# Kernel optimization log

Measured on AMD Instinct MI355X. Metric: run time of the kernel, lower is better.

## Reference

```python
import jax, jax.numpy as jnp
import numpy as np

EPS = 1e-5

def _bn_relu(y, mean, var, scale, bias):
    # y: (b, c, n); eval-mode batchnorm over channel axis, then ReLU
    inv = scale / jnp.sqrt(var + EPS)
    return jax.nn.relu((y - mean[None, :, None]) * inv[None, :, None] + bias[None, :, None])

def setup_inputs() -> dict:
    key = jax.random.key(0)
    ks = jax.random.split(key, 6)
    b, c, n, cr = 4, 256, 4096, 32
    inp = {
        'x': jax.random.normal(ks[0], (b, c, n), jnp.float32),
        'w_q': jax.random.normal(ks[1], (cr, c), jnp.float32) * (1.0 / np.sqrt(c)),
        'w_k': jax.random.normal(ks[2], (cr, c), jnp.float32) * (1.0 / np.sqrt(c)),
        'w_v': jax.random.normal(ks[3], (c, c), jnp.float32) * (1.0 / np.sqrt(c)),
        'bn1_scale': jnp.ones((cr,), jnp.float32), 'bn1_bias': jnp.zeros((cr,), jnp.float32),
        'bn1_mean': jnp.zeros((cr,), jnp.float32), 'bn1_var': jnp.ones((cr,), jnp.float32),
        'bn2_scale': jnp.ones((cr,), jnp.float32), 'bn2_bias': jnp.zeros((cr,), jnp.float32),
        'bn2_mean': jnp.zeros((cr,), jnp.float32), 'bn2_var': jnp.ones((cr,), jnp.float32),
        'bn3_scale': jnp.ones((c,), jnp.float32), 'bn3_bias': jnp.zeros((c,), jnp.float32),
        'bn3_mean': jnp.zeros((c,), jnp.float32), 'bn3_var': jnp.ones((c,), jnp.float32),
        'gamma': jax.random.normal(ks[4], (1,), jnp.float32),
    }
    return inp

def reference(x, w_q, w_k, w_v,
              bn1_scale, bn1_bias, bn1_mean, bn1_var,
              bn2_scale, bn2_bias, bn2_mean, bn2_var,
              bn3_scale, bn3_bias, bn3_mean, bn3_var,
              gamma):
    # x: (b, c, n). Original views as (b, c, n, 1) so width=1, height=n.
    b, c, n = x.shape
    # 1x1 conv == channel matmul, then BN+ReLU
    q = _bn_relu(jnp.einsum('oc,bcn->bon', w_q, x), bn1_mean, bn1_var, bn1_scale, bn1_bias)  # (b, c', n)
    k = _bn_relu(jnp.einsum('oc,bcn->bon', w_k, x), bn2_mean, bn2_var, bn2_scale, bn2_bias)  # (b, c', n)
    v = _bn_relu(jnp.einsum('oc,bcn->bon', w_v, x), bn3_mean, bn3_var, bn3_scale, bn3_bias)  # (b, c, n)
    # energy_H: (b, n, n) with -inf diagonal (self-attention along 'height')
    energy_h = jnp.einsum('bdi,bdj->bij', q, k)
    eye = jnp.eye(n, dtype=bool)
    energy_h = jnp.where(eye[None], -jnp.inf, energy_h)
    # energy_W: width=1 -> per-position self energy (b, n)
    energy_w = jnp.sum(q * k, axis=1)
    # softmax over concat of n H-logits and 1 W-logit
    att = jax.nn.softmax(jnp.concatenate([energy_h, energy_w[..., None]], axis=-1), axis=-1)  # (b, n, n+1)
    att_h = att[..., :n]        # (b, n, n), query i -> key j
    att_w = att[..., n]         # (b, n)
    out_h = jnp.einsum('bcj,bij->bci', v, att_h)   # aggregate values along height
    out_w = v * att_w[:, None, :]                  # width=1 self term
    out = gamma[0] * (out_h + out_w) + x
    return out
```

## Files before the change

### kernel.cpp

```cpp
#include <hip/hip_runtime.h>

#define Bb 4
#define Cc 256
#define Nn 4096
#define CR 32
#define EPS_BN 1e-5f
#define SHIFT2 28.853900817779268f
#define LOG2E  1.4426950408889634f
#define JSPLIT 4
#define JSL (Nn / JSPLIT)
#define TJ 64
#define NTILES (JSL / TJ)

typedef __attribute__((ext_vector_type(8))) short short8;
typedef __attribute__((ext_vector_type(4))) float f32x4;

__device__ inline unsigned int pk2(float a, float b) {
    __bf16 ha = (__bf16)a, hb = (__bf16)b;
    unsigned short ra = __builtin_bit_cast(unsigned short, ha);
    unsigned short rb = __builtin_bit_cast(unsigned short, hb);
    return ((unsigned int)rb << 16) | ra;
}
__device__ inline float blo(unsigned int u) { return __uint_as_float(u << 16); }
__device__ inline float bhi(unsigned int u) { return __uint_as_float(u & 0xffff0000u); }
__device__ inline float ex2(float x) { return __builtin_amdgcn_exp2f(x); }

__global__ __launch_bounds__(256) void qkv_kernel(
    const float* __restrict__ x,
    const float* __restrict__ wq, const float* __restrict__ wk, const float* __restrict__ wv,
    const float* __restrict__ bn1s, const float* __restrict__ bn1b, const float* __restrict__ bn1m, const float* __restrict__ bn1v,
    const float* __restrict__ bn2s, const float* __restrict__ bn2b, const float* __restrict__ bn2m, const float* __restrict__ bn2v,
    const float* __restrict__ bn3s, const float* __restrict__ bn3b, const float* __restrict__ bn3m, const float* __restrict__ bn3v,
    __bf16* __restrict__ Qt, __bf16* __restrict__ Kt, __bf16* __restrict__ Vb)
{
    __shared__ __align__(16) __bf16 F[16384];
    __shared__ __align__(16) float  sXf[4][32 * 40];
    __shared__ __align__(16) __bf16 sXt[4][2][32 * 40];

    const int tid = threadIdx.x;
    const int n0 = blockIdx.x * 128, g = blockIdx.y, b = blockIdx.z;
    const int lane = tid & 63, w = tid >> 6;
    const int l15 = lane & 15, l4 = lane >> 4;

    {
        int r = tid >> 2, q = tid & 3;
        int R = g * 64 + r;
        const float* src = (R < 32) ? (wq + (size_t)R * Cc)
                         : (R < 64) ? (wk + (size_t)(R - 32) * Cc)
                                    : (wv + (size_t)(R - 64) * Cc);
        int mt = r >> 4, l15r = r & 15;
#pragma unroll
        for (int u8 = 0; u8 < 8; ++u8) {
            float4 a = *(const float4*)&src[q * 64 + u8 * 8];
            float4 c2 = *(const float4*)&src[q * 64 + u8 * 8 + 4];
            uint4 p = { pk2(a.x,a.y), pk2(a.z,a.w), pk2(c2.x,c2.y), pk2(c2.z,c2.w) };
            int kc = 2 * q + (u8 >> 2), l4k = u8 & 3;
            *(uint4*)&F[(((kc * 4 + mt) * 64 + l4k * 16 + l15r)) * 8] = p;
        }
    }

    float*  sXfw  = &sXf[w][0];
    __bf16* sXtw0 = &sXt[w][0][0];
    __bf16* sXtw1 = &sXt[w][1][0];

    const int cr = lane >> 3, nq = lane & 7;
    const float* xbase = x + (size_t)(b * Cc + cr) * Nn + n0 + w * 32 + nq * 4;

    float4 xg[4];
#pragma unroll
    for (int it = 0; it < 4; ++it)
        xg[it] = *(const float4*)&xbase[(size_t)(it * 8) * Nn];

    __syncthreads();

    f32x4 acc[4][2];
#pragma unroll
    for (int mt = 0; mt < 4; ++mt)
#pragma unroll
        for (int nt = 0; nt < 2; ++nt) acc[mt][nt] = (f32x4){0.f, 0.f, 0.f, 0.f};

    for (int kc = 0; kc < 8; ++kc) {
#pragma unroll
        for (int it = 0; it < 4; ++it)
            *(float4*)&sXfw[(it * 8 + cr) * 40 + nq * 4] = xg[it];

        if (kc + 1 < 8) {
#pragma unroll
            for (int it = 0; it < 4; ++it)
                xg[it] = *(const float4*)&xbase[(size_t)((kc + 1) * 32 + it * 8) * Nn];
        }

#pragma unroll
        for (int s = 0; s < 2; ++s) {
            int n = lane & 31, c0 = (lane >> 5) * 8 + s * 16;
            float h[8], lo[8];
#pragma unroll
            for (int j = 0; j < 8; ++j) {
                float v = sXfw[(c0 + j) * 40 + n];
                float hh = (float)(__bf16)v;
                h[j] = hh; lo[j] = v - hh;
            }
            uint4 H = { pk2(h[0],h[1]), pk2(h[2],h[3]), pk2(h[4],h[5]), pk2(h[6],h[7]) };
            uint4 L = { pk2(lo[0],lo[1]), pk2(lo[2],lo[3]), pk2(lo[4],lo[5]), pk2(lo[6],lo[7]) };
            *(uint4*)&sXtw0[n * 40 + c0] = H;
            *(uint4*)&sXtw1[n * 40 + c0] = L;
        }

        short8 bh[2], bl[2];
#pragma unroll
        for (int nt = 0; nt < 2; ++nt) {
            bh[nt] = *(const short8*)&sXtw0[(nt * 16 + l15) * 40 + l4 * 8];
            bl[nt] = *(const short8*)&sXtw1[(nt * 16 + l15) * 40 + l4 * 8];
        }
#pragma unroll
        for (int mt = 0; mt < 4; ++mt) {
            short8 af = *(const short8*)&F[((kc * 4 + mt) * 64 + lane) * 8];
#pragma unroll
            for (int nt = 0; nt < 2; ++nt) {
                acc[mt][nt] = __builtin_amdgcn_mfma_f32_16x16x32_bf16(af, bh[nt], acc[mt][nt], 0, 0, 0);
                acc[mt][nt] = __builtin_amdgcn_mfma_f32_16x16x32_bf16(af, bl[nt], acc[mt][nt], 0, 0, 0);
            }
        }
    }

    if (g == 0) {
#pragma unroll
        for (int mt = 0; mt < 4; ++mt) {
            float scl[4], off[4];
#pragma unroll
            for (int r = 0; r < 4; ++r) {
                int R = mt * 16 + l4 * 4 + r;
                float s, o;
                if (R < 32) {
                    s = bn1s[R] * __frsqrt_rn(bn1v[R] + EPS_BN);
                    o = bn1b[R] - bn1m[R] * s;
                } else {
                    int row = R - 32;
                    s = bn2s[row] * __frsqrt_rn(bn2v[row] + EPS_BN);
                    o = bn2b[row] - bn2m[row] * s;
                    s *= LOG2E; o *= LOG2E;
                }
                scl[r] = s; off[r] = o;
            }
            __bf16* dst = (mt < 2) ? Qt : Kt;
            int d0 = (mt & 1) * 16 + l4 * 4;
#pragma unroll
            for (int nt = 0; nt < 2; ++nt) {
                f32x4 a = acc[mt][nt];
                float e0 = fmaxf(fmaf(a.x, scl[0], off[0]), 0.f);
                float e1 = fmaxf(fmaf(a.y, scl[1], off[1]), 0.f);
                float e2 = fmaxf(fmaf(a.z, scl[2], off[2]), 0.f);
                float e3 = fmaxf(fmaf(a.w, scl[3], off[3]), 0.f);
                uint2 p = { pk2(e0, e1), pk2(e2, e3) };
                int n = n0 + w * 32 + nt * 16 + l15;
                *(uint2*)&dst[(size_t)(b * Nn + n) * CR + d0] = p;
            }
        }
    } else {
        __bf16* oT = F;
        __syncthreads();
#pragma unroll
        for (int mt = 0; mt < 4; ++mt) {
            float scl[4], off[4];
#pragma unroll
            for (int r = 0; r < 4; ++r) {
                int row = (g - 1) * 64 + mt * 16 + l4 * 4 + r;
                float s = bn3s[row] * __frsqrt_rn(bn3v[row] + EPS_BN);
                scl[r] = s; off[r] = bn3b[row] - bn3m[row] * s;
            }
#pragma unroll
            for (int nt = 0; nt < 2; ++nt) {
                f32x4 a = acc[mt][nt];
                float e[4];
                e[0] = fmaxf(fmaf(a.x, scl[0], off[0]), 0.f);
                e[1] = fmaxf(fmaf(a.y, scl[1], off[1]), 0.f);
                e[2] = fmaxf(fmaf(a.z, scl[2], off[2]), 0.f);
                e[3] = fmaxf(fmaf(a.w, scl[3], off[3]), 0.f);
                int ncol = w * 32 + nt * 16 + l15;
#pragma unroll
                for (int r = 0; r < 4; ++r)
                    oT[(mt * 16 + l4 * 4 + r) * 136 + ncol] = (__bf16)e[r];
            }
        }
        __syncthreads();
        int rr = tid >> 2, qq = tid & 3;
        size_t vrow = (size_t)(b * Cc + (g - 1) * 64 + rr) * Nn + n0 + qq * 32;
#pragma unroll
        for (int e8 = 0; e8 < 4; ++e8)
            *(uint4*)&Vb[vrow + e8 * 8] = *(const uint4*)&oT[rr * 136 + qq * 32 + e8 * 8];
    }
}

__global__ __launch_bounds__(256) void attn_kernel(
    const __bf16* __restrict__ Qt, const __bf16* __restrict__ Kt,
    const __bf16* __restrict__ Vb,
    __bf16* __restrict__ PO, float* __restrict__ PL)
{
    __shared__ __align__(16) __bf16 sQ[64 * 40];
    __shared__ __align__(16) __bf16 sP[2][64 * 72];
    __shared__ __align__(16) float  sL[4][64];

    const int tid = threadIdx.x, lane = tid & 63, w = tid >> 6;
    const int b = blockIdx.z, js = blockIdx.y, iblk = blockIdx.x;
    const int i0 = iblk * 64;
    const int l15 = lane & 15, l4 = lane >> 4;

    {
        int i = tid >> 2, o = tid & 3;
        *(uint4*)&sQ[i * 40 + o * 8] =
            *(const uint4*)&Qt[(size_t)(b * Nn + i0 + i) * CR + o * 8];
    }
    __syncthreads();
    short8 qf[4];
#pragma unroll
    for (int it = 0; it < 4; ++it)
        qf[it] = *(const short8*)&sQ[(it * 16 + l15) * 40 + l4 * 8];

    f32x4 oacc[16];
#pragma unroll
    for (int z = 0; z < 16; ++z) oacc[z] = (f32x4){0.f, 0.f, 0.f, 0.f};
    float lp[4] = {0.f, 0.f, 0.f, 0.f};

    const size_t jb = (size_t)js * JSL;

    short8 kf = *(const short8*)&Kt[(size_t)(b * Nn + jb + 16 * w + l15) * CR + l4 * 8];

    short8 vf[8];
#pragma unroll
    for (int u = 0; u < 8; ++u) {
        int jh = u >> 2, ct = u & 3;
        int c = w * 64 + ct * 16 + l15;
        vf[u] = *(const short8*)&Vb[(size_t)(b * Cc + c) * Nn + jb + (jh * 4 + l4) * 8];
    }

#pragma unroll
    for (int it = 0; it < 4; ++it) {
        f32x4 c0 = (f32x4){0.f, 0.f, 0.f, 0.f};
        c0 = __builtin_amdgcn_mfma_f32_16x16x32_bf16(kf, qf[it], c0, 0, 0, 0);
        float e0 = ex2(c0.x - SHIFT2), e1 = ex2(c0.y - SHIFT2);
        float e2 = ex2(c0.z - SHIFT2), e3 = ex2(c0.w - SHIFT2);
        lp[it] += (e0 + e1) + (e2 + e3);
        uint2 p2 = { pk2(e0, e1), pk2(e2, e3) };
        *(uint2*)&sP[0][(it * 16 + l15) * 72 + w * 16 + l4 * 4] = p2;
    }
    kf = *(const short8*)&Kt[(size_t)(b * Nn + jb + TJ + 16 * w + l15) * CR + l4 * 8];
    __syncthreads();

    for (int t = 0; t < NTILES; ++t) {
        const size_t j0 = jb + (size_t)t * TJ;
        const __bf16* sPr = &sP[t & 1][0];
        __bf16*       sPn = &sP[(t + 1) & 1][0];

        if (t + 1 < NTILES) {
#pragma unroll
            for (int it = 0; it < 4; ++it) {
                f32x4 c0 = (f32x4){0.f, 0.f, 0.f, 0.f};
                c0 = __builtin_amdgcn_mfma_f32_16x16x32_bf16(kf, qf[it], c0, 0, 0, 0);
                float e0 = ex2(c0.x - SHIFT2), e1 = ex2(c0.y - SHIFT2);
                float e2 = ex2(c0.z - SHIFT2), e3 = ex2(c0.w - SHIFT2);
                lp[it] += (e0 + e1) + (e2 + e3);
                uint2 p2 = { pk2(e0, e1), pk2(e2, e3) };
                *(uint2*)&sPn[(it * 16 + l15) * 72 + w * 16 + l4 * 4] = p2;
            }
        }

        __builtin_amdgcn_s_setprio(1);
#pragma unroll
        for (int jh = 0; jh < 2; ++jh) {
            short8 pf[4];
#pragma unroll
            for (int it = 0; it < 4; ++it)
                pf[it] = *(const short8*)&sPr[(it * 16 + l15) * 72 + jh * 32 + l4 * 8];
#pragma unroll
            for (int ct = 0; ct < 4; ++ct) {
#pragma unroll
                for (int it = 0; it < 4; ++it)
                    oacc[it * 4 + ct] = __builtin_amdgcn_mfma_f32_16x16x32_bf16(
                        pf[it], vf[jh * 4 + ct], oacc[it * 4 + ct], 0, 0, 0);
            }
        }
        __builtin_amdgcn_s_setprio(0);

        if (t + 1 < NTILES) {
#pragma unroll
            for (int u = 0; u < 8; ++u) {
                int jh = u >> 2, ct = u & 3;
                int c = w * 64 + ct * 16 + l15;
                vf[u] = *(const short8*)&Vb[(size_t)(b * Cc + c) * Nn + j0 + TJ + (jh * 4 + l4) * 8];
            }
            if (t + 2 < NTILES)
                kf = *(const short8*)&Kt[(size_t)(b * Nn + j0 + 2 * TJ + 16 * w + l15) * CR + l4 * 8];
            __syncthreads();
        }
    }

#pragma unroll
    for (int it = 0; it < 4; ++it) {
        float v = lp[it];
        v += __shfl_xor(v, 16);
        v += __shfl_xor(v, 32);
        if (lane < 16) sL[w][it * 16 + lane] = v;
    }
    __syncthreads();
    if (tid < 64)
        PL[(size_t)(js * Bb + b) * Nn + i0 + tid] =
            sL[0][tid] + sL[1][tid] + sL[2][tid] + sL[3][tid];

    const size_t base = (size_t)((js * Bb + b) * (Nn / 64) + iblk) * 16384;
#pragma unroll
    for (int it = 0; it < 4; ++it)
#pragma unroll
        for (int ct = 0; ct < 4; ++ct) {
            f32x4 a = oacc[it * 4 + ct];
            uint2 p = { pk2(a.x, a.y), pk2(a.z, a.w) };
            *(uint2*)&PO[base + (size_t)((((w * 4 + it) * 4 + ct) * 64 + lane)) * 4] = p;
        }
}

__global__ __launch_bounds__(256) void reduce_kernel(
    const __bf16* __restrict__ PO, const float* __restrict__ PL,
    const float* __restrict__ x, const float* __restrict__ gamma,
    float* __restrict__ out)
{
    __shared__ __align__(16) float oT[64 * 68];
    __shared__ float sLinv[64];

    const int tid = threadIdx.x;
    const int iblk = blockIdx.x, wq = blockIdx.y, b = blockIdx.z;
    const int i0 = iblk * 64;
    const int lane = tid & 63, ct = tid >> 6, l15 = lane & 15, l4 = lane >> 4;

    if (tid < 64) {
        float l = 0.f;
#pragma unroll
        for (int js = 0; js < JSPLIT; ++js)
            l += PL[(size_t)(js * Bb + b) * Nn + i0 + tid];
        sLinv[tid] = 1.0f / l;
    }

    float o[4][4];
#pragma unroll
    for (int it = 0; it < 4; ++it) {
        o[it][0] = o[it][1] = o[it][2] = o[it][3] = 0.f;
#pragma unroll
        for (int js = 0; js < JSPLIT; ++js) {
            size_t base = (size_t)((js * Bb + b) * (Nn / 64) + iblk) * 16384;
            uint2 v = *(const uint2*)&PO[base + (size_t)((((wq * 4 + it) * 4 + ct) * 64 + lane)) * 4];
            o[it][0] += blo(v.x); o[it][1] += bhi(v.x);
            o[it][2] += blo(v.y); o[it][3] += bhi(v.y);
        }
    }

    const int cl = ct * 16 + l15;
#pragma unroll
    for (int it = 0; it < 4; ++it) {
        float4 t4 = { o[it][0], o[it][1], o[it][2], o[it][3] };
        *(float4*)&oT[cl * 68 + it * 16 + l4 * 4] = t4;
    }
    __syncthreads();

    const float g = gamma[0];
    const int c_l = tid >> 2, icol = (tid & 3) * 16;
    const int cg = wq * 64 + c_l;
    const size_t gb = (size_t)(b * Cc + cg) * Nn + i0 + icol;
#pragma unroll
    for (int k4 = 0; k4 < 4; ++k4) {
        float4 ov = *(const float4*)&oT[c_l * 68 + icol + k4 * 4];
        float4 li = *(const float4*)&sLinv[icol + k4 * 4];
        float4 xv = *(const float4*)&x[gb + k4 * 4];
        float4 res;
        res.x = fmaf(g, ov.x * li.x, xv.x);
        res.y = fmaf(g, ov.y * li.y, xv.y);
        res.z = fmaf(g, ov.z * li.z, xv.z);
        res.w = fmaf(g, ov.w * li.w, xv.w);
        *(float4*)&out[gb + k4 * 4] = res;
    }
}

extern "C" void kernel_launch(void* const* d_in, const int* in_sizes, int n_in,
                              void* d_out, int out_size, void* d_ws, size_t ws_size,
                              hipStream_t stream)
{
    const float* x    = (const float*)d_in[0];
    const float* wq   = (const float*)d_in[1];
    const float* wk   = (const float*)d_in[2];
    const float* wv   = (const float*)d_in[3];
    const float* bn1s = (const float*)d_in[4];
    const float* bn1b = (const float*)d_in[5];
    const float* bn1m = (const float*)d_in[6];
    const float* bn1v = (const float*)d_in[7];
    const float* bn2s = (const float*)d_in[8];
    const float* bn2b = (const float*)d_in[9];
    const float* bn2m = (const float*)d_in[10];
    const float* bn2v = (const float*)d_in[11];
    const float* bn3s = (const float*)d_in[12];
    const float* bn3b = (const float*)d_in[13];
    const float* bn3m = (const float*)d_in[14];
    const float* bn3v = (const float*)d_in[15];
    const float* gmm  = (const float*)d_in[16];
    float* out = (float*)d_out;

    char* ws = (char*)d_ws;
    __bf16* Qt  = (__bf16*)(ws);
    __bf16* Kt  = (__bf16*)(ws + (1u << 20));
    __bf16* Vb  = (__bf16*)(ws + (2u << 20));
    char*   big = ws + (10u << 20);
    __bf16* PO  = (__bf16*)big;
    float*  PL  = (float*)(big + 33554432);

    qkv_kernel<<<dim3(Nn / 128, 5, Bb), 256, 0, stream>>>(
        x, wq, wk, wv,
        bn1s, bn1b, bn1m, bn1v,
        bn2s, bn2b, bn2m, bn2v,
        bn3s, bn3b, bn3m, bn3v,
        Qt, Kt, Vb);

    attn_kernel<<<dim3(Nn / 64, JSPLIT, Bb), 256, 0, stream>>>(Qt, Kt, Vb, PO, PL);

    reduce_kernel<<<dim3(Nn / 64, 4, Bb), 256, 0, stream>>>(PO, PL, x, gmm, out);
}
```

Measured before the change: 211.8 us.

## Pre-pack weights in a separate kernel and widen V projection groups to 128 rows

Adds a small prep kernel that converts the Q/K/V weights to bf16 MFMA fragment layout once, so qkv_kernel reads the fragments directly from global memory instead of each block repacking weights into LDS. The V projection is split into two groups of 128 output rows instead of four of 64, cutting the grid from 5 to 3 groups per tile. This reduces redundant x loads and hi/lo bf16 splitting per block. In exchange it adds a kernel launch, uses more accumulator registers, leaves the Q/K group doing half the work of the V groups, and uses a larger LDS staging buffer.

```diff
diff --git a/kernel.cpp b/kernel.cpp
--- a/kernel.cpp
+++ b/kernel.cpp
@@ -25,39 +25,45 @@
 __device__ inline float bhi(unsigned int u) { return __uint_as_float(u & 0xffff0000u); }
 __device__ inline float ex2(float x) { return __builtin_amdgcn_exp2f(x); }
 
+__global__ __launch_bounds__(256) void prep_w(
+    const float* __restrict__ wq, const float* __restrict__ wk,
+    const float* __restrict__ wv, __bf16* __restrict__ Wf)
+{
+    const int r16 = blockIdx.x;
+    const int tid = threadIdx.x;
+#pragma unroll
+    for (int ss = 0; ss < 2; ++ss) {
+        int s = tid + ss * 256;
+        int kc = s >> 6, lane = s & 63;
+        int R = r16 * 16 + (lane & 15);
+        const float* src = (R < 32) ? (wq + (size_t)R * Cc)
+                         : (R < 64) ? (wk + (size_t)(R - 32) * Cc)
+                                    : (wv + (size_t)(R - 64) * Cc);
+        const float* p = src + kc * 32 + (lane >> 4) * 8;
+        float4 a = *(const float4*)p;
+        float4 c2 = *(const float4*)(p + 4);
+        uint4 pk = { pk2(a.x,a.y), pk2(a.z,a.w), pk2(c2.x,c2.y), pk2(c2.z,c2.w) };
+        *(uint4*)&Wf[(((size_t)r16 * 8 + kc) * 64 + lane) * 8] = pk;
+    }
+}
+
 __global__ __launch_bounds__(256) void qkv_kernel(
-    const float* __restrict__ x,
-    const float* __restrict__ wq, const float* __restrict__ wk, const float* __restrict__ wv,
+    const float* __restrict__ x, const __bf16* __restrict__ Wf,
     const float* __restrict__ bn1s, const float* __restrict__ bn1b, const float* __restrict__ bn1m, const float* __restrict__ bn1v,
     const float* __restrict__ bn2s, const float* __restrict__ bn2b, const float* __restrict__ bn2m, const float* __restrict__ bn2v,
     const float* __restrict__ bn3s, const float* __restrict__ bn3b, const float* __restrict__ bn3m, const float* __restrict__ bn3v,
     __bf16* __restrict__ Qt, __bf16* __restrict__ Kt, __bf16* __restrict__ Vb)
 {
-    __shared__ __align__(16) __bf16 F[16384];
     __shared__ __align__(16) float  sXf[4][32 * 40];
     __shared__ __align__(16) __bf16 sXt[4][2][32 * 40];
+    __shared__ __align__(16) __bf16 oT[128 * 136];
 
     const int tid = threadIdx.x;
     const int n0 = blockIdx.x * 128, g = blockIdx.y, b = blockIdx.z;
     const int lane = tid & 63, w = tid >> 6;
     const int l15 = lane & 15, l4 = lane >> 4;
-
-    {
-        int r = tid >> 2, q = tid & 3;
-        int R = g * 64 + r;
-        const float* src = (R < 32) ? (wq + (size_t)R * Cc)
-                         : (R < 64) ? (wk + (size_t)(R - 32) * Cc)
-                                    : (wv + (size_t)(R - 64) * Cc);
-        int mt = r >> 4, l15r = r & 15;
-#pragma unroll
-        for (int u8 = 0; u8 < 8; ++u8) {
-            float4 a = *(const float4*)&src[q * 64 + u8 * 8];
-            float4 c2 = *(const float4*)&src[q * 64 + u8 * 8 + 4];
-            uint4 p = { pk2(a.x,a.y), pk2(a.z,a.w), pk2(c2.x,c2.y), pk2(c2.z,c2.w) };
-            int kc = 2 * q + (u8 >> 2), l4k = u8 & 3;
-            *(uint4*)&F[(((kc * 4 + mt) * 64 + l4k * 16 + l15r)) * 8] = p;
-        }
-    }
+    const int nmt = (g == 0) ? 4 : 8;
+    const int r16b = (g == 0) ? 0 : 4 + (g - 1) * 8;
 
     float*  sXfw  = &sXf[w][0];
     __bf16* sXtw0 = &sXt[w][0][0];
@@ -71,11 +77,9 @@
     for (int it = 0; it < 4; ++it)
         xg[it] = *(const float4*)&xbase[(size_t)(it * 8) * Nn];
 
-    __syncthreads();
-
-    f32x4 acc[4][2];
-#pragma unroll
-    for (int mt = 0; mt < 4; ++mt)
+    f32x4 acc[8][2];
+#pragma unroll
+    for (int mt = 0; mt < 8; ++mt)
 #pragma unroll
         for (int nt = 0; nt < 2; ++nt) acc[mt][nt] = (f32x4){0.f, 0.f, 0.f, 0.f};
 
@@ -112,13 +116,19 @@
             bh[nt] = *(const short8*)&sXtw0[(nt * 16 + l15) * 40 + l4 * 8];
             bl[nt] = *(const short8*)&sXtw1[(nt * 16 + l15) * 40 + l4 * 8];
         }
-#pragma unroll
-        for (int mt = 0; mt < 4; ++mt) {
-            short8 af = *(const short8*)&F[((kc * 4 + mt) * 64 + lane) * 8];
-#pragma unroll
-            for (int nt = 0; nt < 2; ++nt) {
-                acc[mt][nt] = __builtin_amdgcn_mfma_f32_16x16x32_bf16(af, bh[nt], acc[mt][nt], 0, 0, 0);
-                acc[mt][nt] = __builtin_amdgcn_mfma_f32_16x16x32_bf16(af, bl[nt], acc[mt][nt], 0, 0, 0);
+        short8 af[8];
+#pragma unroll
+        for (int mt = 0; mt < 8; ++mt)
+            if (mt < nmt)
+                af[mt] = *(const short8*)&Wf[(((size_t)(r16b + mt) * 8 + kc) * 64 + lane) * 8];
+#pragma unroll
+        for (int mt = 0; mt < 8; ++mt) {
+            if (mt < nmt) {
+#pragma unroll
+                for (int nt = 0; nt < 2; ++nt) {
+                    acc[mt][nt] = __builtin_amdgcn_mfma_f32_16x16x32_bf16(af[mt], bh[nt], acc[mt][nt], 0, 0, 0);
+                    acc[mt][nt] = __builtin_amdgcn_mfma_f32_16x16x32_bf16(af[mt], bl[nt], acc[mt][nt], 0, 0, 0);
+                }
             }
         }
     }
@@ -157,14 +167,13 @@
             }
         }
     } else {
-        __bf16* oT = F;
-        __syncthreads();
-#pragma unroll
-        for (int mt = 0; mt < 4; ++mt) {
+        const int vr0 = (g - 1) * 128;
+#pragma unroll
+        for (int mt = 0; mt < 8; ++mt) {
             float scl[4], off[4];
 #pragma unroll
             for (int r = 0; r < 4; ++r) {
-                int row = (g - 1) * 64 + mt * 16 + l4 * 4 + r;
+                int row = vr0 + mt * 16 + l4 * 4 + r;
                 float s = bn3s[row] * __frsqrt_rn(bn3v[row] + EPS_BN);
                 scl[r] = s; off[r] = bn3b[row] - bn3m[row] * s;
             }
@@ -183,11 +192,11 @@
             }
         }
         __syncthreads();
-        int rr = tid >> 2, qq = tid & 3;
-        size_t vrow = (size_t)(b * Cc + (g - 1) * 64 + rr) * Nn + n0 + qq * 32;
-#pragma unroll
-        for (int e8 = 0; e8 < 4; ++e8)
-            *(uint4*)&Vb[vrow + e8 * 8] = *(const uint4*)&oT[rr * 136 + qq * 32 + e8 * 8];
+        int rr = tid >> 1, qq = tid & 1;
+        size_t vrow = (size_t)(b * Cc + vr0 + rr) * Nn + n0 + qq * 64;
+#pragma unroll
+        for (int e8 = 0; e8 < 8; ++e8)
+            *(uint4*)&Vb[vrow + e8 * 8] = *(const uint4*)&oT[rr * 136 + qq * 64 + e8 * 8];
     }
 }
 
@@ -407,9 +416,12 @@
     char*   big = ws + (10u << 20);
     __bf16* PO  = (__bf16*)big;
     float*  PL  = (float*)(big + 33554432);
-
-    qkv_kernel<<<dim3(Nn / 128, 5, Bb), 256, 0, stream>>>(
-        x, wq, wk, wv,
+    __bf16* Wf  = (__bf16*)(big + 33554432 + 262144);
+
+    prep_w<<<dim3(20), 256, 0, stream>>>(wq, wk, wv, Wf);
+
+    qkv_kernel<<<dim3(Nn / 128, 3, Bb), 256, 0, stream>>>(
+        x, Wf,
         bn1s, bn1b, bn1m, bn1v,
         bn2s, bn2b, bn2m, bn2v,
         bn3s, bn3b, bn3m, bn3v,
```

After: 204.4 us. -3.5%, faster.
